# Kernel optimization log

Measured on AMD Instinct MI355X. Metric: run time of the kernel, lower is better.

Reference implementation:

```python
import jax, jax.numpy as jnp
import numpy as np

E = 1024
H = 16
D = E // H  # head_dim = 64


def setup_inputs() -> dict:
    key = jax.random.key(0)
    k_x, k_w1, k_b1, k_w2, k_b2 = jax.random.split(key, 5)
    s = 1.0 / np.sqrt(E)
    return {
        "x": jax.random.normal(k_x, (2, 2048, E), dtype=jnp.float32),
        "qkv_w": jax.random.uniform(k_w1, (3 * E, E), jnp.float32, -s, s),
        "qkv_b": jax.random.uniform(k_b1, (3 * E,), jnp.float32, -s, s),
        "out_w": jax.random.uniform(k_w2, (E, E), jnp.float32, -s, s),
        "out_b": jax.random.uniform(k_b2, (E,), jnp.float32, -s, s),
    }


def reference(x, qkv_w, qkv_b, out_w, out_b):
    B, T, _ = x.shape
    # qkv projection (torch Linear: x @ W.T + b)
    qkv = x @ qkv_w.T + qkv_b  # [B, T, 3E]
    q, k, v = jnp.split(qkv, 3, axis=-1)
    # [B, T, E] -> [B, H, T, D]
    def to_heads(t):
        return t.reshape(B, T, H, D).transpose(0, 2, 1, 3)
    q, k, v = to_heads(q), to_heads(k), to_heads(v)
    scale = 1.0 / np.sqrt(D).astype(np.float32)
    scores = jnp.einsum("bhqd,bhkd->bhqk", q, k) * scale  # [B, H, T, T]
    attn = jax.nn.softmax(scores, axis=-1)
    # dropout is identity in eval mode
    out = jnp.einsum("bhqk,bhkd->bhqd", attn, v)  # [B, H, T, D]
    out = out.transpose(0, 2, 1, 3).reshape(B, T, E)
    return out @ out_w.T + out_b
```

## Files before the change

### kernel.cpp

```cpp
#include <hip/hip_runtime.h>

#define TT 2048
#define BB 2
#define EE 1024
#define HH 16
#define DD 64
#define E3 3072
#define NTOK 4096

typedef unsigned short u16;
typedef _Float16 __attribute__((ext_vector_type(8))) half8;
typedef _Float16 __attribute__((ext_vector_type(4))) half4;
typedef __fp16 __attribute__((ext_vector_type(2))) fp16x2;
typedef __attribute__((ext_vector_type(4))) float f32x4;

union PW { half4 h[2]; half8 v; };

__device__ __forceinline__ unsigned f2h(float f) {
    union { _Float16 h; u16 u; } v; v.h = (_Float16)f; return (unsigned)v.u;
}
__device__ __forceinline__ unsigned pkh(float a, float b) {
    union { fp16x2 h; unsigned u; } v;
    v.h = __builtin_amdgcn_cvt_pkrtz(a, b);
    return v.u;
}
__device__ __forceinline__ fp16x2 pk2(float a, float b) {
    return __builtin_amdgcn_cvt_pkrtz(a, b);
}

__device__ __forceinline__ void async_ld16(const u16* g, const u16* l) {
    auto gp = reinterpret_cast<const __attribute__((address_space(1))) unsigned*>(
        reinterpret_cast<uintptr_t>(g));
    auto lp = reinterpret_cast<__attribute__((address_space(3))) unsigned*>(
        reinterpret_cast<uintptr_t>(l));
    __builtin_amdgcn_global_load_lds(gp, lp, 16, 0, 0);
}

#define SYNCVM(N) do {                                                    \
    asm volatile("s_waitcnt vmcnt(" #N ")\n\ts_barrier" ::: "memory");    \
    __builtin_amdgcn_sched_barrier(0);                                    \
} while (0)

__global__ __launch_bounds__(256) void split3(
    const float* __restrict__ x, const float* __restrict__ w1,
    const float* __restrict__ w2,
    u16* __restrict__ xh, u16* __restrict__ w1h, u16* __restrict__ w2h)
{
    const int N1 = (NTOK * EE) / 4;
    const int N2 = N1 + (E3 * EE) / 4;
    int i = blockIdx.x * 256 + threadIdx.x;
    const float* src; u16* dst; int j;
    if (i < N1)      { src = x;  dst = xh;  j = i; }
    else if (i < N2) { src = w1; dst = w1h; j = i - N1; }
    else             { src = w2; dst = w2h; j = i - N2; }
    float4 v = ((const float4*)src)[j];
    *(uint2*)&dst[(size_t)j * 4] = make_uint2(
        f2h(v.x) | (f2h(v.y) << 16), f2h(v.z) | (f2h(v.w) << 16));
}

template <int WMT, bool QSCALE, bool F16OUT>
__global__ __launch_bounds__(256, 3) void gemm_f16(
    const u16* __restrict__ Ag, const u16* __restrict__ Wg,
    const float* __restrict__ bias, void* __restrict__ Cout,
    u16* __restrict__ vtp, int M, int N)
{
    constexpr int BM = WMT * 32;
    constexpr int APASS = BM / 32;
    __shared__ u16 sAB[(BM + 128) * 64];
    u16* sA = sAB;
    u16* sB = sAB + BM * 64;

    const int tid  = threadIdx.x;
    const int lane = tid & 63;
    const int wave = tid >> 6;
    const int quad = lane >> 4;
    const int l16  = lane & 15;
    const int wm = wave >> 1, wn = wave & 1;

    const unsigned nwgx = gridDim.x;
    const unsigned flat = blockIdx.y * nwgx + blockIdx.x;
    const unsigned nwg  = nwgx * gridDim.y;
    const unsigned Wb   = (flat & 7) * (nwg >> 3) + (flat >> 3);
    const int m0 = (int)(Wb / nwgx) * BM;
    const int n0 = (int)(Wb % nwgx) * 128;

    const int srow = tid >> 3;
    const int schk = tid & 7;

    const u16* ag[APASS]; int aldw[APASS];
#pragma unroll
    for (int p = 0; p < APASS; ++p) {
        int row = p * 32 + srow;
        ag[p] = Ag + (size_t)(m0 + row) * EE + ((schk ^ (row & 7)) << 3);
        aldw[p] = (p * 256 + wave * 64) * 8;
    }
    const u16* bg[4]; int bldw[4];
#pragma unroll
    for (int p = 0; p < 4; ++p) {
        int row = p * 32 + srow;
        bg[p] = Wg + (size_t)(n0 + row) * EE + ((schk ^ (row & 7)) << 3);
        bldw[p] = (p * 256 + wave * 64) * 8;
    }

    f32x4 acc[WMT][4];
#pragma unroll
    for (int mt = 0; mt < WMT; ++mt)
#pragma unroll
        for (int nt = 0; nt < 4; ++nt) acc[mt][nt] = (f32x4){0.f, 0.f, 0.f, 0.f};

    for (int k0 = 0; k0 < EE; k0 += 64) {
        __syncthreads();
#pragma unroll
        for (int p = 0; p < APASS; ++p) async_ld16(ag[p] + k0, sA + aldw[p]);
#pragma unroll
        for (int p = 0; p < 4; ++p)    async_ld16(bg[p] + k0, sB + bldw[p]);
        __syncthreads();

        half8 fa[WMT][2], fb[4][2];
#pragma unroll
        for (int mt = 0; mt < WMT; ++mt) {
            int r = wm * (WMT * 16) + mt * 16 + l16;
#pragma unroll
            for (int ks = 0; ks < 2; ++ks)
                fa[mt][ks] = *(const half8*)&sA[r * 64 + (((ks * 4 + quad) ^ (r & 7)) << 3)];
        }
#pragma unroll
        for (int nt = 0; nt < 4; ++nt) {
            int r = wn * 64 + nt * 16 + l16;
#pragma unroll
            for (int ks = 0; ks < 2; ++ks)
                fb[nt][ks] = *(const half8*)&sB[r * 64 + (((ks * 4 + quad) ^ (r & 7)) << 3)];
        }
#pragma unroll
        for (int ks = 0; ks < 2; ++ks)
#pragma unroll
            for (int mt = 0; mt < WMT; ++mt)
#pragma unroll
                for (int nt = 0; nt < 4; ++nt)
                    acc[mt][nt] = __builtin_amdgcn_mfma_f32_16x16x32_f16(
                        fa[mt][ks], fb[nt][ks], acc[mt][nt], 0, 0, 0);
    }

    const float scale = (QSCALE && n0 < EE) ? 0.18033688011112042f : 1.0f;
    float bv[4];
#pragma unroll
    for (int nt = 0; nt < 4; ++nt) bv[nt] = bias[n0 + wn * 64 + nt * 16 + l16];

    if constexpr (F16OUT) {
        if (vtp != nullptr && n0 >= 2 * EE) {
            __syncthreads();
            u16* tile = sAB;
#pragma unroll
            for (int mt = 0; mt < WMT; ++mt)
#pragma unroll
                for (int nt = 0; nt < 4; ++nt) {
                    int c  = wn * 64 + nt * 16 + l16;
                    int ub = (wm * 16 + mt * 4 + quad) ^ ((c & 7) << 1);
                    *(uint2*)&tile[c * 128 + ub * 4] = make_uint2(
                        f2h(acc[mt][nt][0] + bv[nt]) | (f2h(acc[mt][nt][1] + bv[nt]) << 16),
                        f2h(acc[mt][nt][2] + bv[nt]) | (f2h(acc[mt][nt][3] + bv[nt]) << 16));
                }
            __syncthreads();
            const int t8 = tid & 7;
            const int bq = m0 >> 11;
            const int tokb = m0 & (TT - 1);
#pragma unroll
            for (int p = 0; p < 4; ++p) {
                int c  = p * 32 + (tid >> 3);
                int hd = ((n0 - 2 * EE) >> 6) + (c >> 6);
                int d  = c & 63;
                u16* dst = vtp + ((size_t)(bq * HH + hd) * DD + d) * TT
                               + tokb + t8 * 16;
                int x = (c & 7) << 1;
#pragma unroll
                for (int j = 0; j < 2; ++j) {
                    int u = (t8 * 4 + j * 2) ^ x;
                    *(uint4*)(dst + j * 8) = *(const uint4*)&tile[c * 128 + u * 4];
                }
            }
            return;
        }
    }

#pragma unroll
    for (int mt = 0; mt < WMT; ++mt)
#pragma unroll
        for (int nt = 0; nt < 4; ++nt)
#pragma unroll
            for (int r = 0; r < 4; ++r) {
                int rg = m0 + wm * (WMT * 16) + mt * 16 + quad * 4 + r;
                int cg = n0 + wn * 64 + nt * 16 + l16;
                float v = (acc[mt][nt][r] + bv[nt]) * scale;
                if (F16OUT) ((u16*)Cout)[(size_t)rg * N + cg] = (u16)f2h(v);
                else        ((float*)Cout)[(size_t)rg * N + cg] = v;
            }
}

__global__ __launch_bounds__(256, 2) void attn_mfma(
    const u16* __restrict__ qkv, const u16* __restrict__ vt,
    u16* __restrict__ obuf)
{
    __shared__ u16 KB[2][128][64];
    __shared__ u16 VB[2][64][128];

    const int tid  = threadIdx.x;
    const int wave = tid >> 6;
    const int lane = tid & 63;
    const int quad = lane >> 4;
    const int l16  = lane & 15;

    const int q0 = blockIdx.x * 128;
    const int hh = blockIdx.y;
    const int b  = blockIdx.z;

    const int srow  = tid >> 3;
    const int schk  = tid & 7;
    const int vsrow = tid >> 4;
    const int vschk = tid & 15;
    const int ldsw  = wave * 512;

    half8 qb[2][2];
#pragma unroll
    for (int qt = 0; qt < 2; ++qt) {
        int row = q0 + wave * 32 + qt * 16 + l16;
        const u16* qg = qkv + (size_t)(b * TT + row) * E3 + hh * DD;
#pragma unroll
        for (int ks = 0; ks < 2; ++ks)
            qb[qt][ks] = *(const half8*)(qg + ks * 32 + quad * 8);
    }

#pragma unroll
    for (int p = 0; p < 4; ++p) {
        int krow = p * 32 + srow;
        async_ld16(qkv + (size_t)(b * TT + krow) * E3 + EE + hh * DD
                       + ((schk ^ (krow & 7)) << 3),
                   &KB[0][0][0] + p * 2048 + ldsw);
    }
#pragma unroll
    for (int p = 0; p < 4; ++p) {
        int vrow = p * 16 + vsrow;
        async_ld16(vt + ((size_t)(b * HH + hh) * DD + vrow) * TT
                      + ((vschk ^ (vrow & 15)) << 3),
                   &VB[0][0][0] + p * 2048 + ldsw);
    }
    SYNCVM(4);

    const f32x4 Z = {0.f, 0.f, 0.f, 0.f};
    float l_i[2] = {0.f, 0.f};
    f32x4 o[4][2];
#pragma unroll
    for (int dt = 0; dt < 4; ++dt)
#pragma unroll
        for (int qt = 0; qt < 2; ++qt) o[dt][qt] = (f32x4){0.f, 0.f, 0.f, 0.f};

    int cur = 0;
    for (int kt = 0; kt < TT; kt += 128, cur ^= 1) {
        const int ktn = (kt + 128) & (TT - 1);
#pragma unroll
        for (int p = 0; p < 4; ++p) {
            int krow = p * 32 + srow;
            async_ld16(qkv + (size_t)(b * TT + ktn + krow) * E3 + EE + hh * DD
                           + ((schk ^ (krow & 7)) << 3),
                       &KB[cur ^ 1][0][0] + p * 2048 + ldsw);
        }
#pragma unroll
        for (int p = 0; p < 4; ++p) {
            int vrow = p * 16 + vsrow;
            async_ld16(vt + ((size_t)(b * HH + hh) * DD + vrow) * TT + ktn
                          + ((vschk ^ (vrow & 15)) << 3),
                       &VB[cur ^ 1][0][0] + p * 2048 + ldsw);
        }

        PW pw[2][4];
#pragma unroll
        for (int kg = 0; kg < 8; ++kg) {
            int r0 = kg * 16 + l16;
            half8 kf0 = *(const half8*)&KB[cur][r0][((quad)     ^ (r0 & 7)) << 3];
            half8 kf1 = *(const half8*)&KB[cur][r0][((4 + quad) ^ (r0 & 7)) << 3];
#pragma unroll
            for (int qt = 0; qt < 2; ++qt) {
                f32x4 t = __builtin_amdgcn_mfma_f32_16x16x32_f16(kf0, qb[qt][0], Z, 0, 0, 0);
                f32x4 s = __builtin_amdgcn_mfma_f32_16x16x32_f16(kf1, qb[qt][1], t, 0, 0, 0);
                float p0 = __builtin_amdgcn_exp2f(s[0]);
                float p1 = __builtin_amdgcn_exp2f(s[1]);
                float p2 = __builtin_amdgcn_exp2f(s[2]);
                float p3 = __builtin_amdgcn_exp2f(s[3]);
                l_i[qt] += (p0 + p1) + (p2 + p3);
                union { fp16x2 h[2]; half4 v; } u;
                u.h[0] = pk2(p0, p1);
                u.h[1] = pk2(p2, p3);
                pw[qt][kg >> 1].h[kg & 1] = u.v;
            }
        }

        SYNCVM(8);

#pragma unroll
        for (int w = 0; w < 4; ++w) {
            const int cl  = w * 4 + (quad >> 1);
            const int sub = (quad & 1) << 2;
#pragma unroll
            for (int dt = 0; dt < 4; ++dt) {
                int vr = dt * 16 + l16;
                PW va;
                va.h[0] = *(const half4*)&VB[cur][vr][((cl       ^ l16) << 3) + sub];
                va.h[1] = *(const half4*)&VB[cur][vr][(((cl + 2) ^ l16) << 3) + sub];
                o[dt][0] = __builtin_amdgcn_mfma_f32_16x16x32_f16(va.v, pw[0][w].v, o[dt][0], 0, 0, 0);
                o[dt][1] = __builtin_amdgcn_mfma_f32_16x16x32_f16(va.v, pw[1][w].v, o[dt][1], 0, 0, 0);
            }
        }

        SYNCVM(4);
    }

    float inv[2];
#pragma unroll
    for (int qt = 0; qt < 2; ++qt) {
        float l = l_i[qt];
        l += __shfl_xor(l, 16, 64);
        l += __shfl_xor(l, 32, 64);
        inv[qt] = 1.f / l;
    }
#pragma unroll
    for (int qt = 0; qt < 2; ++qt) {
        size_t base = (size_t)(b * TT + q0 + wave * 32 + qt * 16 + l16) * EE + hh * DD;
#pragma unroll
        for (int dt = 0; dt < 4; ++dt) {
            unsigned hv[4];
#pragma unroll
            for (int r = 0; r < 4; ++r) hv[r] = f2h(o[dt][qt][r] * inv[qt]);
            *(uint2*)&obuf[base + dt * 16 + quad * 4] =
                make_uint2(hv[0] | (hv[1] << 16), hv[2] | (hv[3] << 16));
        }
    }
}

extern "C" void kernel_launch(void* const* d_in, const int* in_sizes, int n_in,
                              void* d_out, int out_size, void* d_ws, size_t ws_size,
                              hipStream_t stream)
{
    const float* x     = (const float*)d_in[0];
    const float* qkv_w = (const float*)d_in[1];
    const float* qkv_b = (const float*)d_in[2];
    const float* out_w = (const float*)d_in[3];
    const float* out_b = (const float*)d_in[4];
    float* out = (float*)d_out;

    const size_t NX  = (size_t)NTOK * EE;
    const size_t NW1 = (size_t)E3 * EE;
    const size_t NW2 = (size_t)EE * EE;
    const size_t NQ  = (size_t)NTOK * E3;

    u16* ws   = (u16*)d_ws;
    u16* x_h  = ws;
    u16* w1h  = ws + NX;
    u16* w2h  = w1h + NW1;
    u16* qkvb = w2h + NW2;
    u16* vtb  = qkvb + NQ;

    split3<<<dim3((unsigned)((NX + NW1 + NW2) / 4 / 256)), 256, 0, stream>>>(
        x, qkv_w, out_w, x_h, w1h, w2h);

    gemm_f16<4, true, true><<<dim3(E3 / 128, NTOK / 128), 256, 0, stream>>>(
        x_h, w1h, qkv_b, (void*)qkvb, vtb, NTOK, E3);

    attn_mfma<<<dim3(TT / 128, HH, BB), 256, 0, stream>>>(qkvb, vtb, x_h);

    gemm_f16<2, false, false><<<dim3(EE / 128, NTOK / 64), 256, 0, stream>>>(
        x_h, w2h, out_b, (void*)out, nullptr, NTOK, EE);
}
```

Baseline: 178.8 us.

## Split attention key dimension across wave pairs with 64-query tiles and LDS reduction

Each wave now handles 64 query rows and half of every 128-key tile, instead of 32 query rows and the full tile. Each K/V fragment read from LDS therefore feeds twice as many MFMAs, cutting LDS read traffic per FLOP. The two key halves are merged at the end through shared memory, which reuses the K/V buffer space. This costs more accumulator registers (o[4][4], qb[4][2]), which may hurt occupancy under launch_bounds(256,2), plus extra barriers and a reduction step.

```diff
diff --git a/kernel.cpp b/kernel.cpp
--- a/kernel.cpp
+++ b/kernel.cpp
@@ -200,14 +200,18 @@
     const u16* __restrict__ qkv, const u16* __restrict__ vt,
     u16* __restrict__ obuf)
 {
-    __shared__ u16 KB[2][128][64];
-    __shared__ u16 VB[2][64][128];
+    __shared__ __align__(16) char SM[65536];
+    u16* KBp = (u16*)SM;
+    u16* VBp = (u16*)(SM + 32768);
+    float* ORDf = (float*)SM;
 
     const int tid  = threadIdx.x;
     const int wave = tid >> 6;
     const int lane = tid & 63;
     const int quad = lane >> 4;
     const int l16  = lane & 15;
+    const int qh   = wave >> 1;
+    const int kh   = wave & 1;
 
     const int q0 = blockIdx.x * 128;
     const int hh = blockIdx.y;
@@ -219,10 +223,10 @@
     const int vschk = tid & 15;
     const int ldsw  = wave * 512;
 
-    half8 qb[2][2];
-#pragma unroll
-    for (int qt = 0; qt < 2; ++qt) {
-        int row = q0 + wave * 32 + qt * 16 + l16;
+    half8 qb[4][2];
+#pragma unroll
+    for (int qt = 0; qt < 4; ++qt) {
+        int row = q0 + qh * 64 + qt * 16 + l16;
         const u16* qg = qkv + (size_t)(b * TT + row) * E3 + hh * DD;
 #pragma unroll
         for (int ks = 0; ks < 2; ++ks)
@@ -234,24 +238,24 @@
         int krow = p * 32 + srow;
         async_ld16(qkv + (size_t)(b * TT + krow) * E3 + EE + hh * DD
                        + ((schk ^ (krow & 7)) << 3),
-                   &KB[0][0][0] + p * 2048 + ldsw);
+                   KBp + p * 2048 + ldsw);
     }
 #pragma unroll
     for (int p = 0; p < 4; ++p) {
         int vrow = p * 16 + vsrow;
         async_ld16(vt + ((size_t)(b * HH + hh) * DD + vrow) * TT
                       + ((vschk ^ (vrow & 15)) << 3),
-                   &VB[0][0][0] + p * 2048 + ldsw);
+                   VBp + p * 2048 + ldsw);
     }
     SYNCVM(4);
 
     const f32x4 Z = {0.f, 0.f, 0.f, 0.f};
-    float l_i[2] = {0.f, 0.f};
-    f32x4 o[4][2];
+    float l_i[4] = {0.f, 0.f, 0.f, 0.f};
+    f32x4 o[4][4];
 #pragma unroll
     for (int dt = 0; dt < 4; ++dt)
 #pragma unroll
-        for (int qt = 0; qt < 2; ++qt) o[dt][qt] = (f32x4){0.f, 0.f, 0.f, 0.f};
+        for (int qt = 0; qt < 4; ++qt) o[dt][qt] = (f32x4){0.f, 0.f, 0.f, 0.f};
 
     int cur = 0;
     for (int kt = 0; kt < TT; kt += 128, cur ^= 1) {
@@ -261,24 +265,25 @@
             int krow = p * 32 + srow;
             async_ld16(qkv + (size_t)(b * TT + ktn + krow) * E3 + EE + hh * DD
                            + ((schk ^ (krow & 7)) << 3),
-                       &KB[cur ^ 1][0][0] + p * 2048 + ldsw);
+                       KBp + (cur ^ 1) * 8192 + p * 2048 + ldsw);
         }
 #pragma unroll
         for (int p = 0; p < 4; ++p) {
             int vrow = p * 16 + vsrow;
             async_ld16(vt + ((size_t)(b * HH + hh) * DD + vrow) * TT + ktn
                           + ((vschk ^ (vrow & 15)) << 3),
-                       &VB[cur ^ 1][0][0] + p * 2048 + ldsw);
-        }
-
-        PW pw[2][4];
-#pragma unroll
-        for (int kg = 0; kg < 8; ++kg) {
-            int r0 = kg * 16 + l16;
-            half8 kf0 = *(const half8*)&KB[cur][r0][((quad)     ^ (r0 & 7)) << 3];
-            half8 kf1 = *(const half8*)&KB[cur][r0][((4 + quad) ^ (r0 & 7)) << 3];
-#pragma unroll
-            for (int qt = 0; qt < 2; ++qt) {
+                       VBp + (cur ^ 1) * 8192 + p * 2048 + ldsw);
+        }
+
+        PW pw[4][2];
+#pragma unroll
+        for (int kg = 0; kg < 4; ++kg) {
+            int r0 = kh * 64 + kg * 16 + l16;
+            const u16* kb = KBp + cur * 8192 + r0 * 64;
+            half8 kf0 = *(const half8*)&kb[((quad)     ^ (r0 & 7)) << 3];
+            half8 kf1 = *(const half8*)&kb[((4 + quad) ^ (r0 & 7)) << 3];
+#pragma unroll
+            for (int qt = 0; qt < 4; ++qt) {
                 f32x4 t = __builtin_amdgcn_mfma_f32_16x16x32_f16(kf0, qb[qt][0], Z, 0, 0, 0);
                 f32x4 s = __builtin_amdgcn_mfma_f32_16x16x32_f16(kf1, qb[qt][1], t, 0, 0, 0);
                 float p0 = __builtin_amdgcn_exp2f(s[0]);
@@ -296,41 +301,65 @@
         SYNCVM(8);
 
 #pragma unroll
-        for (int w = 0; w < 4; ++w) {
-            const int cl  = w * 4 + (quad >> 1);
+        for (int w = 0; w < 2; ++w) {
+            const int cl  = kh * 8 + w * 4 + (quad >> 1);
             const int sub = (quad & 1) << 2;
 #pragma unroll
             for (int dt = 0; dt < 4; ++dt) {
                 int vr = dt * 16 + l16;
+                const u16* vb = VBp + cur * 8192 + vr * 128;
                 PW va;
-                va.h[0] = *(const half4*)&VB[cur][vr][((cl       ^ l16) << 3) + sub];
-                va.h[1] = *(const half4*)&VB[cur][vr][(((cl + 2) ^ l16) << 3) + sub];
-                o[dt][0] = __builtin_amdgcn_mfma_f32_16x16x32_f16(va.v, pw[0][w].v, o[dt][0], 0, 0, 0);
-                o[dt][1] = __builtin_amdgcn_mfma_f32_16x16x32_f16(va.v, pw[1][w].v, o[dt][1], 0, 0, 0);
+                va.h[0] = *(const half4*)&vb[((cl       ^ l16) << 3) + sub];
+                va.h[1] = *(const half4*)&vb[(((cl + 2) ^ l16) << 3) + sub];
+#pragma unroll
+                for (int qt = 0; qt < 4; ++qt)
+                    o[dt][qt] = __builtin_amdgcn_mfma_f32_16x16x32_f16(
+                        va.v, pw[qt][w].v, o[dt][qt], 0, 0, 0);
             }
         }
 
         SYNCVM(4);
     }
 
-    float inv[2];
-#pragma unroll
-    for (int qt = 0; qt < 2; ++qt) {
+    float lw[4];
+#pragma unroll
+    for (int qt = 0; qt < 4; ++qt) {
         float l = l_i[qt];
         l += __shfl_xor(l, 16, 64);
         l += __shfl_xor(l, 32, 64);
-        inv[qt] = 1.f / l;
-    }
-#pragma unroll
-    for (int qt = 0; qt < 2; ++qt) {
-        size_t base = (size_t)(b * TT + q0 + wave * 32 + qt * 16 + l16) * EE + hh * DD;
-#pragma unroll
-        for (int dt = 0; dt < 4; ++dt) {
-            unsigned hv[4];
-#pragma unroll
-            for (int r = 0; r < 4; ++r) hv[r] = f2h(o[dt][qt][r] * inv[qt]);
-            *(uint2*)&obuf[base + dt * 16 + quad * 4] =
-                make_uint2(hv[0] | (hv[1] << 16), hv[2] | (hv[3] << 16));
+        lw[qt] = l;
+    }
+
+    __syncthreads();
+
+    if (kh == 1) {
+#pragma unroll
+        for (int qt = 0; qt < 4; ++qt) {
+            int q = qh * 64 + qt * 16 + l16;
+#pragma unroll
+            for (int dt = 0; dt < 4; ++dt)
+                *(f32x4*)&ORDf[q * 68 + dt * 16 + quad * 4] = o[dt][qt];
+            if (quad == 0) ORDf[8704 + q] = lw[qt];
+        }
+    }
+    __syncthreads();
+
+    if (kh == 0) {
+#pragma unroll
+        for (int qt = 0; qt < 4; ++qt) {
+            int q = qh * 64 + qt * 16 + l16;
+            float inv = 1.f / (lw[qt] + ORDf[8704 + q]);
+            size_t base = (size_t)(b * TT + q0 + q) * EE + hh * DD;
+#pragma unroll
+            for (int dt = 0; dt < 4; ++dt) {
+                f32x4 pv = *(const f32x4*)&ORDf[q * 68 + dt * 16 + quad * 4];
+                unsigned hv[4];
+#pragma unroll
+                for (int r = 0; r < 4; ++r)
+                    hv[r] = f2h((o[dt][qt][r] + pv[r]) * inv);
+                *(uint2*)&obuf[base + dt * 16 + quad * 4] =
+                    make_uint2(hv[0] | (hv[1] << 16), hv[2] | (hv[3] << 16));
+            }
         }
     }
 }
```

Result: no change. 176.4 us (-1.4%).
